# Performance work log

Measured on AMD Instinct MI355X. Metric: run time of the kernel, lower is better.

Reference implementation:

```python
import jax, jax.numpy as jnp
import numpy as np

D_MODEL = 2048
NUM_HEADS = 16
NUM_KV_HEADS = 4
HEAD_DIM = D_MODEL // NUM_HEADS  # 128
THETA = 10000.0


def _rotate_half(x):
    # interleaved rotate: pairs (x0,x1) -> (-x1, x0)
    x1 = x[..., ::2]
    x2 = x[..., 1::2]
    return jnp.stack((-x2, x1), axis=-1).reshape(x.shape)


def _rope_cos_sin(seq_len, dtype):
    inv_freq = 1.0 / (THETA ** (jnp.arange(0, HEAD_DIM, 2, dtype=jnp.float32) / HEAD_DIM))
    pos = jnp.arange(seq_len, dtype=jnp.float32)
    freqs = pos[:, None] * inv_freq[None, :]            # [S, HD/2]
    emb = jnp.repeat(freqs, 2, axis=-1)                  # [S, HD] interleaved
    return jnp.cos(emb).astype(dtype), jnp.sin(emb).astype(dtype)


def setup_inputs() -> dict:
    key = jax.random.key(0)
    ks = jax.random.split(key, 5)
    B, S = 2, 2048
    x = jax.random.normal(ks[0], (B, S, D_MODEL), dtype=jnp.float32)
    scale = 0.02
    wq = jax.random.normal(ks[1], (D_MODEL, NUM_HEADS * HEAD_DIM), dtype=jnp.float32) * scale
    wk = jax.random.normal(ks[2], (D_MODEL, NUM_KV_HEADS * HEAD_DIM), dtype=jnp.float32) * scale
    wv = jax.random.normal(ks[3], (D_MODEL, NUM_KV_HEADS * HEAD_DIM), dtype=jnp.float32) * scale
    wo = jax.random.normal(ks[4], (D_MODEL, D_MODEL), dtype=jnp.float32) * scale
    return {"x": x, "wq": wq, "wk": wk, "wv": wv, "wo": wo}


def reference(x, wq, wk, wv, wo):
    B, S, _ = x.shape
    q = (x @ wq).reshape(B, S, NUM_HEADS, HEAD_DIM).transpose(0, 2, 1, 3)      # [B,H,S,D]
    k = (x @ wk).reshape(B, S, NUM_KV_HEADS, HEAD_DIM).transpose(0, 2, 1, 3)   # [B,KV,S,D]
    v = (x @ wv).reshape(B, S, NUM_KV_HEADS, HEAD_DIM).transpose(0, 2, 1, 3)

    cos, sin = _rope_cos_sin(S, q.dtype)
    cos = cos[None, None]  # [1,1,S,HD]
    sin = sin[None, None]
    q = q * cos + _rotate_half(q) * sin
    k = k * cos + _rotate_half(k) * sin

    reps = NUM_HEADS // NUM_KV_HEADS
    k = jnp.repeat(k, reps, axis=1)  # [B,H,S,D]
    v = jnp.repeat(v, reps, axis=1)

    scale = 1.0 / jnp.sqrt(jnp.asarray(HEAD_DIM, dtype=q.dtype))
    scores = jnp.einsum('bhqd,bhkd->bhqk', q, k) * scale
    causal = jnp.tril(jnp.ones((S, S), dtype=bool))
    scores = jnp.where(causal[None, None], scores, jnp.finfo(scores.dtype).min)
    attn = jax.nn.softmax(scores, axis=-1)
    y = jnp.einsum('bhqk,bhkd->bhqd', attn, v)            # [B,H,S,D]
    y = y.transpose(0, 2, 1, 3).reshape(B, S, NUM_HEADS * HEAD_DIM)
    return y @ wo
```

## Files before the change

kernel.cpp:

```cpp
#include <hip/hip_runtime.h>
#include <hip/hip_bf16.h>
#include <stdint.h>

typedef __hip_bfloat16 bf16;
typedef __attribute__((ext_vector_type(8))) short short8;
typedef __attribute__((ext_vector_type(4))) float f32x4;

#define D_MODEL 2048
#define NHEADS 16
#define NKV 4
#define HD 128
#define BATCH 2
#define SEQ 2048
#define NTOK (BATCH*SEQ)
#define QKV_N 3072
#define QSCALE 0.08838834764831845f

__global__ __launch_bounds__(256) void trig_kernel(float2* __restrict__ tab) {
    int idx = blockIdx.x * 256 + threadIdx.x;
    int s = idx >> 6, i = idx & 63;
    double inv_freq = pow(10000.0, -(double)i / 64.0);
    double sn, cs;
    sincos((double)s * inv_freq, &sn, &cs);
    tab[idx] = make_float2((float)cs, (float)sn);
}

__global__ __launch_bounds__(256) void conv8(const float* __restrict__ in,
                                             bf16* __restrict__ out, int n8) {
    int idx = blockIdx.x * 256 + threadIdx.x;
    if (idx >= n8) return;
    const float4* p = (const float4*)(in + (size_t)idx * 8);
    float4 a = p[0], b = p[1];
    union { short8 v; bf16 e[8]; } u;
    u.e[0] = __float2bfloat16(a.x); u.e[1] = __float2bfloat16(a.y);
    u.e[2] = __float2bfloat16(a.z); u.e[3] = __float2bfloat16(a.w);
    u.e[4] = __float2bfloat16(b.x); u.e[5] = __float2bfloat16(b.y);
    u.e[6] = __float2bfloat16(b.z); u.e[7] = __float2bfloat16(b.w);
    *(short8*)(out + (size_t)idx * 8) = u.v;
}

#define TILE_LD 68
__global__ __launch_bounds__(256) void ct64(const float* __restrict__ in,
                                            bf16* __restrict__ out, int K, int N) {
    __shared__ float tile[64 * TILE_LD];
    int n0 = blockIdx.x * 64, k0 = blockIdx.y * 64;
    int t = threadIdx.x;
#pragma unroll
    for (int i = 0; i < 4; ++i) {
        int idx = t + 256 * i;
        int r = idx >> 4;
        int c4 = (idx & 15) * 4;
        *(float4*)&tile[r * TILE_LD + c4] = *(const float4*)(in + (size_t)(k0 + r) * N + n0 + c4);
    }
    __syncthreads();
#pragma unroll
    for (int i = 0; i < 2; ++i) {
        int idx = t + 256 * i;
        int n = idx >> 3;
        int kc = (idx & 7) * 8;
        union { short8 v; bf16 e[8]; } u;
#pragma unroll
        for (int j = 0; j < 8; ++j) u.e[j] = __float2bfloat16(tile[(kc + j) * TILE_LD + n]);
        *(short8*)(out + (size_t)(n0 + n) * K + k0 + kc) = u.v;
    }
}

__global__ __launch_bounds__(256) void vt64(const bf16* __restrict__ qkvb,
                                            bf16* __restrict__ vT) {
    __shared__ bf16 tile[64 * 72];
    int vd0 = blockIdx.x * 64, s0 = blockIdx.y * 64, b = blockIdx.z;
    int t = threadIdx.x;
#pragma unroll
    for (int i = 0; i < 2; ++i) {
        int idx = t + 256 * i;
        int r = idx >> 3;
        int c8 = (idx & 7) * 8;
        *(int4*)&tile[r * 72 + c8] =
            *(const int4*)(qkvb + (size_t)(b * SEQ + s0 + r) * QKV_N + 2560 + vd0 + c8);
    }
    __syncthreads();
#pragma unroll
    for (int i = 0; i < 2; ++i) {
        int idx = t + 256 * i;
        int vd = idx >> 3;
        int s8 = (idx & 7) * 8;
        union { short8 v; bf16 e[8]; } u;
#pragma unroll
        for (int j = 0; j < 8; ++j) u.e[j] = tile[(s8 + j) * 72 + vd];
        *(short8*)(vT + (size_t)(b * 512 + vd0 + vd) * 2048 + s0 + s8) = u.v;
    }
}

template <typename OutT, bool ROPE>
__global__ __launch_bounds__(256) void gemm_bt(const bf16* __restrict__ A,
                                               const bf16* __restrict__ Bt,
                                               OutT* __restrict__ C, int M, int N, int K,
                                               const float2* __restrict__ trig) {
    __shared__ bf16 As[128 * 32];
    __shared__ bf16 Bs[128 * 32];
    const int m0 = blockIdx.y * 128, n0 = blockIdx.x * 128;
    const int tid = threadIdx.x;
    const int wave = tid >> 6, lane = tid & 63;
    const int wr = wave >> 1, wc = wave & 1;
    const int l15 = lane & 15, g = lane >> 4;
    const int srow = lane >> 2;
    const int sk8 = (lane & 3) * 8;
    f32x4 acc[4][4] = {};

    for (int k0 = 0; k0 < K; k0 += 32) {
        __syncthreads();
#pragma unroll
        for (int i = 0; i < 2; ++i) {
            int chunk = wave * 2 + i;
            const bf16* ga = A + (size_t)(m0 + chunk * 16 + srow) * K + k0 + sk8;
            bf16* la = As + chunk * 512 + lane * 8;
            __builtin_amdgcn_global_load_lds((const __attribute__((address_space(1))) void*)ga,
                                             (__attribute__((address_space(3))) void*)la, 16, 0, 0);
            const bf16* gb = Bt + (size_t)(n0 + chunk * 16 + srow) * K + k0 + sk8;
            bf16* lb = Bs + chunk * 512 + lane * 8;
            __builtin_amdgcn_global_load_lds((const __attribute__((address_space(1))) void*)gb,
                                             (__attribute__((address_space(3))) void*)lb, 16, 0, 0);
        }
        __syncthreads();
        short8 af[4], bfr[4];
#pragma unroll
        for (int mi = 0; mi < 4; ++mi)
            af[mi] = *(const short8*)&As[(wr * 64 + mi * 16 + l15) * 32 + g * 8];
#pragma unroll
        for (int ni = 0; ni < 4; ++ni)
            bfr[ni] = *(const short8*)&Bs[(wc * 64 + ni * 16 + l15) * 32 + g * 8];
#pragma unroll
        for (int mi = 0; mi < 4; ++mi)
#pragma unroll
            for (int ni = 0; ni < 4; ++ni)
                acc[mi][ni] = __builtin_amdgcn_mfma_f32_16x16x32_bf16(af[mi], bfr[ni], acc[mi][ni], 0, 0, 0);
    }
#pragma unroll
    for (int mi = 0; mi < 4; ++mi)
#pragma unroll
        for (int ni = 0; ni < 4; ++ni) {
            int row = m0 + wr * 64 + mi * 16 + g * 4;
            int col = n0 + wc * 64 + ni * 16 + l15;
#pragma unroll
            for (int r = 0; r < 4; ++r) {
                float v = acc[mi][ni][r];
                if constexpr (ROPE) {
                    float partner = __shfl_xor(v, 1);
                    if (col < 2560) {
                        int s = (row + r) & (SEQ - 1);
                        int i2 = (col & 127) >> 1;
                        float2 t = trig[s * 64 + i2];
                        v = (col & 1) ? (v * t.x + partner * t.y)
                                      : (v * t.x - partner * t.y);
                    }
                    if (col < 2048) v *= QSCALE;
                }
                if constexpr (__is_same(OutT, float))
                    C[(size_t)(row + r) * N + col] = v;
                else
                    C[(size_t)(row + r) * N + col] = __float2bfloat16(v);
            }
        }
}

#define PL_LD 72
__global__ __launch_bounds__(256) void attn5(const bf16* __restrict__ qkv,
                                             const bf16* __restrict__ vT,
                                             bf16* __restrict__ y) {
    const int bx = blockIdx.x, h = blockIdx.y, b = blockIdx.z;
    const int kvh = h >> 2;
    const int tid = threadIdx.x, wave = tid >> 6, lane = tid & 63;
    const int l15 = lane & 15, g = lane >> 4;
    __shared__ bf16 Ks[64 * 128];
    __shared__ bf16 Vt[128 * 64];
    __shared__ bf16 Pl[4][16 * PL_LD];
    bf16* plw = Pl[0] + wave * 16 * PL_LD;

    for (int half = 0; half < 2; ++half) {
        const int qt = half ? (31 - bx) : bx;
        const int qrow0 = qt * 64 + wave * 16;
        short8 qf[4];
        {
            const bf16* qp = qkv + (size_t)(b * SEQ + qrow0 + l15) * QKV_N + h * HD + g * 8;
#pragma unroll
            for (int c = 0; c < 4; ++c) qf[c] = *(const short8*)(qp + c * 32);
        }
        f32x4 acc[8] = {};
        float m_[4], lsum[4];
#pragma unroll
        for (int r = 0; r < 4; ++r) { m_[r] = -3.0e38f; lsum[r] = 0.f; }

        const int diag_kv0 = qt * 64;
        for (int kv0 = 0; kv0 <= diag_kv0; kv0 += 64) {
#pragma unroll
            for (int i = 0; i < 4; ++i) {
                int cidx = tid + 256 * i;
                int key = cidx >> 4, j = cidx & 15;
                const bf16* gk = qkv + (size_t)(b * SEQ + kv0 + key) * QKV_N + D_MODEL
                               + kvh * HD + 8 * (j ^ (key & 7));
                __builtin_amdgcn_global_load_lds(
                    (const __attribute__((address_space(1))) void*)gk,
                    (__attribute__((address_space(3))) void*)(Ks + cidx * 8), 16, 0, 0);
                int d = cidx >> 3, j2 = cidx & 7;
                const bf16* gv = vT + (size_t)(b * 512 + kvh * HD + d) * 2048
                               + kv0 + 8 * (j2 ^ (d & 7));
                __builtin_amdgcn_global_load_lds(
                    (const __attribute__((address_space(1))) void*)gv,
                    (__attribute__((address_space(3))) void*)(Vt + cidx * 8), 16, 0, 0);
            }
            __syncthreads();

            f32x4 sc[4];
#pragma unroll
            for (int ct = 0; ct < 4; ++ct) {
                sc[ct] = (f32x4){0.f, 0.f, 0.f, 0.f};
                int key = ct * 16 + l15;
                int ksw = (key & 7) << 3;
#pragma unroll
                for (int c = 0; c < 4; ++c) {
                    short8 kf = *(const short8*)&Ks[key * 128 + ((c * 32 + g * 8) ^ ksw)];
                    sc[ct] = __builtin_amdgcn_mfma_f32_16x16x32_bf16(qf[c], kf, sc[ct], 0, 0, 0);
                }
            }
            if (kv0 == diag_kv0) {
                int qbase = qrow0 + g * 4;
#pragma unroll
                for (int ct = 0; ct < 4; ++ct) {
                    int key = kv0 + ct * 16 + l15;
#pragma unroll
                    for (int r = 0; r < 4; ++r)
                        if (key > qbase + r) sc[ct][r] = -3.0e38f;
                }
            }
#pragma unroll
            for (int r = 0; r < 4; ++r) {
                float mx = fmaxf(fmaxf(sc[0][r], sc[1][r]), fmaxf(sc[2][r], sc[3][r]));
#pragma unroll
                for (int o = 1; o < 16; o <<= 1) mx = fmaxf(mx, __shfl_xor(mx, o));
                if (mx > m_[r]) {
                    float alpha = __expf(m_[r] - mx);
                    m_[r] = mx;
                    lsum[r] *= alpha;
#pragma unroll
                    for (int nt = 0; nt < 8; ++nt) acc[nt][r] *= alpha;
                }
                float p0 = __expf(sc[0][r] - m_[r]);
                float p1 = __expf(sc[1][r] - m_[r]);
                float p2 = __expf(sc[2][r] - m_[r]);
                float p3 = __expf(sc[3][r] - m_[r]);
                int row = g * 4 + r;
                plw[row * PL_LD + l15]      = __float2bfloat16(p0);
                plw[row * PL_LD + 16 + l15] = __float2bfloat16(p1);
                plw[row * PL_LD + 32 + l15] = __float2bfloat16(p2);
                plw[row * PL_LD + 48 + l15] = __float2bfloat16(p3);
                lsum[r] += (p0 + p1) + (p2 + p3);
            }
            short8 pf0 = *(const short8*)&plw[l15 * PL_LD + g * 8];
            short8 pf1 = *(const short8*)&plw[l15 * PL_LD + 32 + g * 8];
#pragma unroll
            for (int nt = 0; nt < 8; ++nt) {
                int d = nt * 16 + l15;
                int dsw = (d & 7) << 3;
                short8 vf0 = *(const short8*)&Vt[d * 64 + ((g * 8) ^ dsw)];
                short8 vf1 = *(const short8*)&Vt[d * 64 + ((32 + g * 8) ^ dsw)];
                acc[nt] = __builtin_amdgcn_mfma_f32_16x16x32_bf16(pf0, vf0, acc[nt], 0, 0, 0);
                acc[nt] = __builtin_amdgcn_mfma_f32_16x16x32_bf16(pf1, vf1, acc[nt], 0, 0, 0);
            }
            __syncthreads();
        }
        float linv[4];
#pragma unroll
        for (int r = 0; r < 4; ++r) {
            float ls = lsum[r];
#pragma unroll
            for (int o = 1; o < 16; o <<= 1) ls += __shfl_xor(ls, o);
            linv[r] = 1.0f / ls;
        }
        int qrow = qrow0 + g * 4;
#pragma unroll
        for (int nt = 0; nt < 8; ++nt) {
            int d = nt * 16 + l15;
#pragma unroll
            for (int r = 0; r < 4; ++r)
                y[(size_t)(b * SEQ + qrow + r) * D_MODEL + h * HD + d] =
                    __float2bfloat16(acc[nt][r] * linv[r]);
        }
    }
}

extern "C" void kernel_launch(void* const* d_in, const int* in_sizes, int n_in,
                              void* d_out, int out_size, void* d_ws, size_t ws_size,
                              hipStream_t stream) {
    const float* x  = (const float*)d_in[0];
    const float* wq = (const float*)d_in[1];
    const float* wk = (const float*)d_in[2];
    const float* wv = (const float*)d_in[3];
    const float* wo = (const float*)d_in[4];

    bf16*   qkvb  = (bf16*)d_ws;
    bf16*   ybb   = (bf16*)d_ws + (size_t)NTOK * 3072;
    bf16*   woT   = (bf16*)d_ws + (size_t)NTOK * 3072 + (size_t)NTOK * D_MODEL;
    bf16*   xb    = (bf16*)d_out;
    bf16*   wqkvT = (bf16*)d_out + (size_t)NTOK * D_MODEL;
    float2* trig  = (float2*)((bf16*)d_out + (size_t)NTOK * D_MODEL + (size_t)QKV_N * D_MODEL);
    bf16*   vT    = (bf16*)d_out;
    float*  outf  = (float*)d_out;

    conv8<<<dim3(NTOK * D_MODEL / (256 * 8)), 256, 0, stream>>>(x, xb, NTOK * D_MODEL / 8);
    ct64<<<dim3(32, 32), 256, 0, stream>>>(wq, wqkvT, 2048, 2048);
    ct64<<<dim3(8, 32), 256, 0, stream>>>(wk, wqkvT + (size_t)2048 * 2048, 2048, 512);
    ct64<<<dim3(8, 32), 256, 0, stream>>>(wv, wqkvT + (size_t)2560 * 2048, 2048, 512);
    ct64<<<dim3(32, 32), 256, 0, stream>>>(wo, woT, 2048, 2048);
    trig_kernel<<<dim3(SEQ * 64 / 256), 256, 0, stream>>>(trig);

    gemm_bt<bf16, true><<<dim3(QKV_N / 128, NTOK / 128), 256, 0, stream>>>(
        xb, wqkvT, qkvb, NTOK, QKV_N, D_MODEL, trig);

    vt64<<<dim3(8, 32, BATCH), 256, 0, stream>>>(qkvb, vT);

    attn5<<<dim3(16, NHEADS, BATCH), 256, 0, stream>>>(qkvb, vT, ybb);

    gemm_bt<float, false><<<dim3(D_MODEL / 128, NTOK / 128), 256, 0, stream>>>(
        ybb, woT, outf, NTOK, D_MODEL, D_MODEL, nullptr);
}
```

Before: 272.1 us.

## Double-buffer K/V tiles in attention with async prefetch and MFMA priority

The attention kernel now keeps two LDS buffers for K and V. It issues the global-to-LDS loads for the next 64-key tile right after the barrier, then computes on the current tile, which removes the second barrier per iteration and overlaps loads with MFMA work. Global addresses are computed once and advanced by a pointer increment instead of being recomputed each iteration. s_setprio raises wave priority around the MFMA blocks. Doubling the K/V LDS footprint may lower the number of resident blocks per CU.

```diff
diff --git a/kernel.cpp b/kernel.cpp
--- a/kernel.cpp
+++ b/kernel.cpp
@@ -164,17 +164,32 @@
 }
 
 #define PL_LD 72
-__global__ __launch_bounds__(256) void attn5(const bf16* __restrict__ qkv,
+__global__ __launch_bounds__(256) void attn6(const bf16* __restrict__ qkv,
                                              const bf16* __restrict__ vT,
                                              bf16* __restrict__ y) {
     const int bx = blockIdx.x, h = blockIdx.y, b = blockIdx.z;
     const int kvh = h >> 2;
     const int tid = threadIdx.x, wave = tid >> 6, lane = tid & 63;
     const int l15 = lane & 15, g = lane >> 4;
-    __shared__ bf16 Ks[64 * 128];
-    __shared__ bf16 Vt[128 * 64];
+    __shared__ bf16 Ks[2][64 * 128];
+    __shared__ bf16 Vt[2][128 * 64];
     __shared__ bf16 Pl[4][16 * PL_LD];
     bf16* plw = Pl[0] + wave * 16 * PL_LD;
+
+#define STAGE(buf)                                                                       \
+    _Pragma("unroll")                                                                    \
+    for (int i_ = 0; i_ < 4; ++i_) {                                                     \
+        int cidx_ = tid + 256 * i_;                                                      \
+        __builtin_amdgcn_global_load_lds(                                                \
+            (const __attribute__((address_space(1))) void*)gk[i_],                       \
+            (__attribute__((address_space(3))) void*)(Ks[buf] + cidx_ * 8), 16, 0, 0);   \
+        __builtin_amdgcn_global_load_lds(                                                \
+            (const __attribute__((address_space(1))) void*)gv[i_],                       \
+            (__attribute__((address_space(3))) void*)(Vt[buf] + cidx_ * 8), 16, 0, 0);   \
+    }
+#define ADVANCE()                                                                        \
+    _Pragma("unroll")                                                                    \
+    for (int i_ = 0; i_ < 4; ++i_) { gk[i_] += 64 * QKV_N; gv[i_] += 64; }
 
     for (int half = 0; half < 2; ++half) {
         const int qt = half ? (31 - bx) : bx;
@@ -190,27 +205,28 @@
 #pragma unroll
         for (int r = 0; r < 4; ++r) { m_[r] = -3.0e38f; lsum[r] = 0.f; }
 
+        const bf16* gk[4];
+        const bf16* gv[4];
+#pragma unroll
+        for (int i = 0; i < 4; ++i) {
+            int cidx = tid + 256 * i;
+            int key = cidx >> 4, j = cidx & 15;
+            gk[i] = qkv + (size_t)(b * SEQ + key) * QKV_N + D_MODEL + kvh * HD + 8 * (j ^ (key & 7));
+            int d = cidx >> 3, j2 = cidx & 7;
+            gv[i] = vT + (size_t)(b * 512 + kvh * HD + d) * 2048 + 8 * (j2 ^ (d & 7));
+        }
+
         const int diag_kv0 = qt * 64;
-        for (int kv0 = 0; kv0 <= diag_kv0; kv0 += 64) {
-#pragma unroll
-            for (int i = 0; i < 4; ++i) {
-                int cidx = tid + 256 * i;
-                int key = cidx >> 4, j = cidx & 15;
-                const bf16* gk = qkv + (size_t)(b * SEQ + kv0 + key) * QKV_N + D_MODEL
-                               + kvh * HD + 8 * (j ^ (key & 7));
-                __builtin_amdgcn_global_load_lds(
-                    (const __attribute__((address_space(1))) void*)gk,
-                    (__attribute__((address_space(3))) void*)(Ks + cidx * 8), 16, 0, 0);
-                int d = cidx >> 3, j2 = cidx & 7;
-                const bf16* gv = vT + (size_t)(b * 512 + kvh * HD + d) * 2048
-                               + kv0 + 8 * (j2 ^ (d & 7));
-                __builtin_amdgcn_global_load_lds(
-                    (const __attribute__((address_space(1))) void*)gv,
-                    (__attribute__((address_space(3))) void*)(Vt + cidx * 8), 16, 0, 0);
-            }
+        int cur = 0;
+        STAGE(0);
+        ADVANCE();
+        for (int kv0 = 0;; kv0 += 64) {
             __syncthreads();
+            const bool last = (kv0 == diag_kv0);
+            if (!last) { STAGE(cur ^ 1); ADVANCE(); }
 
             f32x4 sc[4];
+            __builtin_amdgcn_s_setprio(1);
 #pragma unroll
             for (int ct = 0; ct < 4; ++ct) {
                 sc[ct] = (f32x4){0.f, 0.f, 0.f, 0.f};
@@ -218,11 +234,12 @@
                 int ksw = (key & 7) << 3;
 #pragma unroll
                 for (int c = 0; c < 4; ++c) {
-                    short8 kf = *(const short8*)&Ks[key * 128 + ((c * 32 + g * 8) ^ ksw)];
+                    short8 kf = *(const short8*)&Ks[cur][key * 128 + ((c * 32 + g * 8) ^ ksw)];
                     sc[ct] = __builtin_amdgcn_mfma_f32_16x16x32_bf16(qf[c], kf, sc[ct], 0, 0, 0);
                 }
             }
-            if (kv0 == diag_kv0) {
+            __builtin_amdgcn_s_setprio(0);
+            if (last) {
                 int qbase = qrow0 + g * 4;
 #pragma unroll
                 for (int ct = 0; ct < 4; ++ct) {
@@ -257,16 +274,19 @@
             }
             short8 pf0 = *(const short8*)&plw[l15 * PL_LD + g * 8];
             short8 pf1 = *(const short8*)&plw[l15 * PL_LD + 32 + g * 8];
+            __builtin_amdgcn_s_setprio(1);
 #pragma unroll
             for (int nt = 0; nt < 8; ++nt) {
                 int d = nt * 16 + l15;
                 int dsw = (d & 7) << 3;
-                short8 vf0 = *(const short8*)&Vt[d * 64 + ((g * 8) ^ dsw)];
-                short8 vf1 = *(const short8*)&Vt[d * 64 + ((32 + g * 8) ^ dsw)];
+                short8 vf0 = *(const short8*)&Vt[cur][d * 64 + ((g * 8) ^ dsw)];
+                short8 vf1 = *(const short8*)&Vt[cur][d * 64 + ((32 + g * 8) ^ dsw)];
                 acc[nt] = __builtin_amdgcn_mfma_f32_16x16x32_bf16(pf0, vf0, acc[nt], 0, 0, 0);
                 acc[nt] = __builtin_amdgcn_mfma_f32_16x16x32_bf16(pf1, vf1, acc[nt], 0, 0, 0);
             }
-            __syncthreads();
+            __builtin_amdgcn_s_setprio(0);
+            if (last) break;
+            cur ^= 1;
         }
         float linv[4];
 #pragma unroll
@@ -285,7 +305,10 @@
                 y[(size_t)(b * SEQ + qrow + r) * D_MODEL + h * HD + d] =
                     __float2bfloat16(acc[nt][r] * linv[r]);
         }
-    }
+        __syncthreads();
+    }
+#undef STAGE
+#undef ADVANCE
 }
 
 extern "C" void kernel_launch(void* const* d_in, const int* in_sizes, int n_in,
@@ -318,7 +341,7 @@
 
     vt64<<<dim3(8, 32, BATCH), 256, 0, stream>>>(qkvb, vT);
 
-    attn5<<<dim3(16, NHEADS, BATCH), 256, 0, stream>>>(qkvb, vT, ybb);
+    attn6<<<dim3(16, NHEADS, BATCH), 256, 0, stream>>>(qkvb, vT, ybb);
 
     gemm_bt<float, false><<<dim3(D_MODEL / 128, NTOK / 128), 256, 0, stream>>>(
         ybb, woT, outf, NTOK, D_MODEL, D_MODEL, nullptr);
```

Measured after the change: 320.4 us. +17.7%, slower.
